# Kernel optimization log

Hardware: AMD Instinct MI355X
Metric: run time of the kernel (lower is better)

## Reference

```python
import jax, jax.numpy as jnp
import numpy as np

HID = 512
HEADS = 8
HEAD_DIM = HID // HEADS
BS, SEQ = 4, 2048


def setup_inputs() -> dict:
    key = jax.random.key(0)
    ks = jax.random.split(key, 12)
    s = 0.02
    return {
        "query": jax.random.normal(ks[0], (BS, SEQ, HID), jnp.float32),
        "key": jax.random.normal(ks[1], (BS, SEQ, HID), jnp.float32),
        "value": jax.random.normal(ks[2], (BS, SEQ, HID), jnp.float32),
        "query_mask": jnp.ones((BS, SEQ), dtype=bool),
        "key_mask": jnp.ones((BS, SEQ), dtype=bool),
        "Wq": jax.random.normal(ks[3], (HID, HID), jnp.float32) * s,
        "bq": jnp.zeros((HID,), jnp.float32),
        "Wk": jax.random.normal(ks[4], (HID, HID), jnp.float32) * s,
        "bk": jnp.zeros((HID,), jnp.float32),
        "Wv": jax.random.normal(ks[5], (HID, HID), jnp.float32) * s,
        "bv": jnp.zeros((HID,), jnp.float32),
        "Wo": jax.random.normal(ks[6], (HID, HID), jnp.float32) * s,
        "bo": jnp.zeros((HID,), jnp.float32),
    }


def _mha(query, key, value, query_mask, key_mask, Wq, bq, Wk, bk, Wv, bv, Wo, bo):
    bs, q_len, _ = query.shape
    k_len = key.shape[1]
    scale = jnp.sqrt(jnp.asarray(HEAD_DIM, query.dtype))

    def proj(x, W, b):  # nn.Linear: x @ W^T + b, then split heads -> [b,h,s,d]
        y = jnp.einsum('bse,fe->bsf', x, W) + b
        return y.reshape(bs, -1, HEADS, HEAD_DIM).transpose(0, 2, 1, 3)

    q = proj(query, Wq, bq)
    k = proj(key, Wk, bk)
    v = proj(value, Wv, bv)

    energy = jnp.einsum('bhqd,bhkd->bhqk', q, k) / scale  # [b,h,q,k]
    neg = -jnp.finfo(energy.dtype).max

    pad_mask = query_mask[:, None, :, None] & key_mask[:, None, None, :]
    energy = jnp.where(pad_mask, energy, neg)

    # causal: mask positions where q_idx < k_idx
    causal = jnp.arange(q_len)[:, None] < jnp.arange(k_len)[None, :]
    energy = jnp.where(causal[None, None], neg, energy)

    attn = jax.nn.softmax(energy, axis=-1)  # dropout p=0.0 -> identity
    x = jnp.einsum('bhqk,bhkd->bhqd', attn, v)
    x = x.transpose(0, 2, 1, 3).reshape(bs, q_len, HID)
    return jnp.einsum('bse,fe->bsf', x, Wo) + bo


def reference(query, key, value, query_mask, key_mask, Wq, bq, Wk, bk, Wv, bv, Wo, bo):
    return _mha(query, key, value, query_mask, key_mask, Wq, bq, Wk, bk, Wv, bv, Wo, bo)
```

## Files before the change

### kernel.cpp

```cpp
#include <hip/hip_runtime.h>
#include <hip/hip_bf16.h>

#define DEVI __device__ __forceinline__

typedef __attribute__((ext_vector_type(4)))  float f32x4;
typedef __attribute__((ext_vector_type(16))) float f32x16;
typedef __attribute__((ext_vector_type(8)))  short bf16x8;

constexpr int BS    = 4;
constexpr int SEQ   = 2048;
constexpr int HID   = 512;
constexpr int HEADS = 8;
constexpr int HD    = 64;
constexpr int M     = BS * SEQ;

constexpr float QSCALE = 0.125f * 1.4426950408889634f;
constexpr float M0 = 4.0f;

DEVI ushort f2bf(float f) {
    union { float f; unsigned u; } a; a.f = f;
    unsigned r = a.u + 0x7fffu + ((a.u >> 16) & 1u);
    return (ushort)(r >> 16);
}

DEVI f32x4 mfma16(bf16x8 a, bf16x8 b, f32x4 c) {
    return __builtin_amdgcn_mfma_f32_16x16x32_bf16(a, b, c, 0, 0, 0);
}
DEVI f32x16 mfma32(bf16x8 a, bf16x8 b, f32x16 c) {
    return __builtin_amdgcn_mfma_f32_32x32x16_bf16(a, b, c, 0, 0, 0);
}

DEVI void gl_lds16(const ushort* g, ushort* l) {
    __builtin_amdgcn_global_load_lds(
        (const __attribute__((address_space(1))) void*)g,
        (__attribute__((address_space(3))) void*)l,
        16, 0, 0);
}

DEVI unsigned cvtpk(float lo, float hi) {
    unsigned r;
    asm("v_cvt_pk_bf16_f32 %0, %1, %2" : "=v"(r) : "v"(lo), "v"(hi));
    return r;
}

DEVI void cvt_store(ushort* dst, float4 a, float4 b) {
    union { unsigned u[4]; bf16x8 v; } p;
    p.u[0] = cvtpk(a.x, a.y); p.u[1] = cvtpk(a.z, a.w);
    p.u[2] = cvtpk(b.x, b.y); p.u[3] = cvtpk(b.z, b.w);
    *(bf16x8*)dst = p.v;
}

__global__ void cast_w(const float* __restrict__ wq, const float* __restrict__ wk,
                       const float* __restrict__ wv, const float* __restrict__ wo,
                       ushort* __restrict__ oq, ushort* __restrict__ ok,
                       ushort* __restrict__ ov, ushort* __restrict__ oo)
{
    const int NW4 = HID * HID / 4;
    int i = blockIdx.x * blockDim.x + threadIdx.x;
    const int a = i >> 16, j = i & (NW4 - 1);
    const float* src = (a == 0) ? wq : (a == 1) ? wk : (a == 2) ? wv : wo;
    ushort* dst = (a == 0) ? oq : (a == 1) ? ok : (a == 2) ? ov : oo;
    float4 f = ((const float4*)src)[j];
    ushort4 u;
    u.x = f2bf(f.x); u.y = f2bf(f.y); u.z = f2bf(f.z); u.w = f2bf(f.w);
    ((ushort4*)dst)[j] = u;
}

template<bool AF32>
DEVI void gemm_core(const void* __restrict__ Ain, const ushort* __restrict__ W,
                    const float* __restrict__ bias, void* __restrict__ out,
                    float scale, int mode, ushort* sh)
{
    constexpr int BK = 32, NK = HID / BK;
    ushort* lA = sh;
    ushort* lB = sh + 12288;
    const int tid  = threadIdx.x;
    const int lane = tid & 63, w = tid >> 6;
    const int wm = w >> 1, wn = w & 1;
    const int l15 = lane & 15, lg = lane >> 4;
    const int m0 = blockIdx.x * 128, n0 = blockIdx.y * 128;
    const int fr = lane & 15;
    const int fc = (lane >> 4) * 8;

    const ushort* Ab  = (const ushort*)Ain;
    const float*  Af  = (const float*)Ain;
    const ushort* Ar0 = Ab + (size_t)(m0 + 32 * w + fr) * HID + fc;
    const ushort* Ar1 = Ab + (size_t)(m0 + 32 * w + 16 + fr) * HID + fc;
    const float*  Af0 = Af + (size_t)(m0 + 32 * w + fr) * HID + fc;
    const float*  Af1 = Af + (size_t)(m0 + 32 * w + 16 + fr) * HID + fc;
    const ushort* Wr0 = W + (size_t)(n0 + 32 * w + fr) * HID + fc;
    const ushort* Wr1 = W + (size_t)(n0 + 32 * w + 16 + fr) * HID + fc;

    ushort* ldsA0 = lA;
    ushort* wrA0  = lA + (2 * w) * 512 + lane * 8;
    ushort* wrA1  = lA + (2 * w + 1) * 512 + lane * 8;

    f32x4 acc[4][4];
    #pragma unroll
    for (int i = 0; i < 4; i++)
        #pragma unroll
        for (int n = 0; n < 4; n++) acc[i][n] = f32x4{0.f, 0.f, 0.f, 0.f};

    float4 rA[2][4];

    if constexpr (AF32) {
        rA[0][0] = *(const float4*)(Af0);
        rA[0][1] = *(const float4*)(Af0 + 4);
        rA[0][2] = *(const float4*)(Af1);
        rA[0][3] = *(const float4*)(Af1 + 4);
        gl_lds16(Wr0, lB + (2 * w) * 512);
        gl_lds16(Wr1, lB + (2 * w + 1) * 512);
        rA[1][0] = *(const float4*)(Af0 + BK);
        rA[1][1] = *(const float4*)(Af0 + BK + 4);
        rA[1][2] = *(const float4*)(Af1 + BK);
        rA[1][3] = *(const float4*)(Af1 + BK + 4);
        gl_lds16(Wr0 + BK, lB + 4096 + (2 * w) * 512);
        gl_lds16(Wr1 + BK, lB + 4096 + (2 * w + 1) * 512);
        asm volatile("s_waitcnt vmcnt(6)" ::: "memory");
        cvt_store(wrA0, rA[0][0], rA[0][1]);
        cvt_store(wrA1, rA[0][2], rA[0][3]);
        asm volatile("s_waitcnt lgkmcnt(0)" ::: "memory");
        asm volatile("s_barrier" ::: "memory");
    } else {
        #pragma unroll
        for (int kk = 0; kk < 2; kk++) {
            gl_lds16(Ar0 + kk * BK, lA + kk * 4096 + (2 * w) * 512);
            gl_lds16(Ar1 + kk * BK, lA + kk * 4096 + (2 * w + 1) * 512);
            gl_lds16(Wr0 + kk * BK, lB + kk * 4096 + (2 * w) * 512);
            gl_lds16(Wr1 + kk * BK, lB + kk * 4096 + (2 * w + 1) * 512);
        }
        asm volatile("s_waitcnt vmcnt(4)" ::: "memory");
        asm volatile("s_barrier" ::: "memory");
    }

    #pragma unroll
    for (int k = 0; k < NK; ++k) {
        const int cb = k % 3;
        const int nb = (k + 2) % 3;
        const int wb = (k + 1) % 3;
        ushort* lAc = lA + cb * 4096;
        ushort* lBc = lB + cb * 4096;

        if (k + 2 < NK) {
            if constexpr (AF32) {
                rA[k & 1][0] = *(const float4*)(Af0 + (k + 2) * BK);
                rA[k & 1][1] = *(const float4*)(Af0 + (k + 2) * BK + 4);
                rA[k & 1][2] = *(const float4*)(Af1 + (k + 2) * BK);
                rA[k & 1][3] = *(const float4*)(Af1 + (k + 2) * BK + 4);
            } else {
                gl_lds16(Ar0 + (k + 2) * BK, lA + nb * 4096 + (2 * w) * 512);
                gl_lds16(Ar1 + (k + 2) * BK, lA + nb * 4096 + (2 * w + 1) * 512);
            }
            gl_lds16(Wr0 + (k + 2) * BK, lB + nb * 4096 + (2 * w) * 512);
            gl_lds16(Wr1 + (k + 2) * BK, lB + nb * 4096 + (2 * w + 1) * 512);
        }

        bf16x8 af[4], bfr[4];
        #pragma unroll
        for (int i = 0; i < 4; i++)
            af[i] = *(const bf16x8*)(lAc + (wm * 4 + i) * 512 + lane * 8);
        #pragma unroll
        for (int n = 0; n < 4; n++)
            bfr[n] = *(const bf16x8*)(lBc + (wn * 4 + n) * 512 + lane * 8);
        __builtin_amdgcn_s_setprio(1);
        #pragma unroll
        for (int i = 0; i < 4; i++)
            #pragma unroll
            for (int n = 0; n < 4; n++)
                acc[i][n] = mfma16(af[i], bfr[n], acc[i][n]);
        __builtin_amdgcn_s_setprio(0);

        if (k + 1 < NK) {
            if constexpr (AF32) {
                if (k + 2 < NK) asm volatile("s_waitcnt vmcnt(6)" ::: "memory");
                else            asm volatile("s_waitcnt vmcnt(0)" ::: "memory");
                cvt_store(wrA0 + wb * 4096, rA[(k + 1) & 1][0], rA[(k + 1) & 1][1]);
                cvt_store(wrA1 + wb * 4096, rA[(k + 1) & 1][2], rA[(k + 1) & 1][3]);
                asm volatile("s_waitcnt lgkmcnt(0)" ::: "memory");
            } else {
                if (k + 2 < NK) asm volatile("s_waitcnt vmcnt(4)" ::: "memory");
                else            asm volatile("s_waitcnt vmcnt(0)" ::: "memory");
            }
            asm volatile("s_barrier" ::: "memory");
        }
    }

    if (mode == 3) {
        #pragma unroll
        for (int i = 0; i < 4; i++) {
            #pragma unroll
            for (int n = 0; n < 4; n++) {
                const int col = n0 + wn * 64 + n * 16 + l15;
                const float bb = bias[col];
                const int rbase = m0 + wm * 64 + i * 16 + lg * 4;
                #pragma unroll
                for (int jj = 0; jj < 4; jj++) {
                    ((float*)out)[(size_t)(rbase + jj) * HID + col] =
                        (acc[i][n][jj] + bb) * scale;
                }
            }
        }
        return;
    }

    __syncthreads();
    #pragma unroll
    for (int i = 0; i < 4; i++) {
        const int tloc = wm * 2 + (i >> 1);
        #pragma unroll
        for (int n = 0; n < 4; n++) {
            const int col = n0 + wn * 64 + n * 16 + l15;
            const float bb = bias[col];
            #pragma unroll
            for (int jj = 0; jj < 4; jj++) {
                const ushort u = f2bf((acc[i][n][jj] + bb) * scale);
                int inner;
                if (mode == 0) {
                    const int l31r = (i & 1) * 16 + lg * 4 + jj;
                    inner = n * 512 + ((l15 >> 3) * 32 + l31r) * 8 + (l15 & 7);
                } else {
                    inner = ((n >> 1) * 2 + (i & 1)) * 512 +
                            ((lg & 1) * 32 + (n & 1) * 16 + l15) * 8 +
                            jj + (lg >> 1) * 4;
                }
                sh[(wn * 4 + tloc) * 2048 + inner] = u;
            }
        }
    }
    __syncthreads();
    const int b  = m0 >> 11;
    const int t0 = (m0 & (SEQ - 1)) >> 5;
    ushort* og = (ushort*)out;
    #pragma unroll
    for (int c = 0; c < 8; c++) {
        const int hl = c >> 2, tl = c & 3;
        const int bh = b * HEADS + (n0 >> 6) + hl;
        *(bf16x8*)(og + (((size_t)bh * 64 + t0 + tl) * 4) * 512 + tid * 8) =
            *(const bf16x8*)(sh + c * 2048 + tid * 8);
    }
}

__global__ __launch_bounds__(256, 3)
void gemm_qkv(const float* __restrict__ Xq, const float* __restrict__ Xk,
              const float* __restrict__ Xv,
              const ushort* __restrict__ Wq, const ushort* __restrict__ Wk,
              const ushort* __restrict__ Wv,
              const float* __restrict__ bq, const float* __restrict__ bk,
              const float* __restrict__ bv,
              ushort* __restrict__ Qf, ushort* __restrict__ Kf,
              ushort* __restrict__ Vf)
{
    __shared__ ushort sh[24576];
    const int z = blockIdx.z;
    const float* A = z == 0 ? Xq : z == 1 ? Xk : Xv;
    const ushort* W = z == 0 ? Wq : z == 1 ? Wk : Wv;
    const float* bias = z == 0 ? bq : z == 1 ? bk : bv;
    void* out = z == 0 ? (void*)Qf : z == 1 ? (void*)Kf : (void*)Vf;
    gemm_core<true>(A, W, bias, out, z == 0 ? QSCALE : 1.0f, z == 2 ? 2 : 0, sh);
}

__global__ __launch_bounds__(256, 3)
void gemm_o(const ushort* __restrict__ ctx, const ushort* __restrict__ Wo,
            const float* __restrict__ bo, float* __restrict__ out)
{
    __shared__ ushort sh[24576];
    gemm_core<false>(ctx, Wo, bo, out, 1.0f, 3, sh);
}

__global__ __launch_bounds__(512)
void attn8(const ushort* __restrict__ Qf, const ushort* __restrict__ Kf,
           const ushort* __restrict__ Vf, ushort* __restrict__ ctx)
{
    __shared__ float part[2][4][16][64];
    __shared__ float pl[2][4][32];

    const int tid  = threadIdx.x;
    const int lane = tid & 63, w = tid >> 6;
    const int qsel = w >> 2, s = w & 3;
    const int l31 = lane & 31, hi = lane >> 5;

    const int bid = blockIdx.x;
    const int bh  = bid & 31;
    const int j   = bid >> 5;
    const int qt  = (62 - 2 * j) + qsel;
    const int qb  = qt * 32;

    const ushort* Qb = Qf + ((size_t)bh * 64 + qt) * 2048;
    const ushort* Kb = Kf + (size_t)bh * 64 * 2048;
    const ushort* Vb = Vf + (size_t)bh * 64 * 2048;

    bf16x8 qf[4];
    #pragma unroll
    for (int ds = 0; ds < 4; ds++)
        qf[ds] = *(const bf16x8*)(Qb + ds * 512 + lane * 8);

    f32x16 acc0 = {}, acc1 = {};
    float lrun = 0.f;

    bf16x8 kf[4] = {}, va[4] = {};
    if (s <= qt) {
        const ushort* kp = Kb + (size_t)s * 2048 + lane * 8;
        const ushort* vp = Vb + (size_t)s * 2048 + lane * 8;
        #pragma unroll
        for (int ds = 0; ds < 4; ds++) {
            kf[ds] = *(const bf16x8*)(kp + ds * 512);
            va[ds] = *(const bf16x8*)(vp + ds * 512);
        }
    }

    for (int t = s; t <= qt; t += 4) {
        f32x16 sc = {};
        __builtin_amdgcn_s_setprio(1);
        #pragma unroll
        for (int ds = 0; ds < 4; ds++)
            sc = mfma32(kf[ds], qf[ds], sc);
        __builtin_amdgcn_s_setprio(0);

        bf16x8 kfn[4], van[4];
        {
            const int tn = (t + 4 <= qt) ? t + 4 : t;
            const ushort* kp = Kb + (size_t)tn * 2048 + lane * 8;
            const ushort* vp = Vb + (size_t)tn * 2048 + lane * 8;
            #pragma unroll
            for (int ds = 0; ds < 4; ds++) {
                kfn[ds] = *(const bf16x8*)(kp + ds * 512);
                van[ds] = *(const bf16x8*)(vp + ds * 512);
            }
        }

        if (t == qt) {
            #pragma unroll
            for (int r = 0; r < 16; r++) {
                const int kvrow = (r & 3) + 8 * (r >> 2) + 4 * hi;
                sc[r] = (kvrow > l31) ? -3e38f : sc[r];
            }
        }

        float e[16];
        #pragma unroll
        for (int r = 0; r < 16; r++)
            e[r] = __builtin_amdgcn_exp2f(sc[r] - M0);
        float es0 = (e[0] + e[1]) + (e[2] + e[3]);
        float es1 = (e[4] + e[5]) + (e[6] + e[7]);
        float es2 = (e[8] + e[9]) + (e[10] + e[11]);
        float es3 = (e[12] + e[13]) + (e[14] + e[15]);
        lrun += (es0 + es1) + (es2 + es3);

        union { unsigned u[4]; bf16x8 v; } pb0, pb1;
        pb0.u[0] = cvtpk(e[0],  e[1]);  pb0.u[1] = cvtpk(e[2],  e[3]);
        pb0.u[2] = cvtpk(e[4],  e[5]);  pb0.u[3] = cvtpk(e[6],  e[7]);
        pb1.u[0] = cvtpk(e[8],  e[9]);  pb1.u[1] = cvtpk(e[10], e[11]);
        pb1.u[2] = cvtpk(e[12], e[13]); pb1.u[3] = cvtpk(e[14], e[15]);

        __builtin_amdgcn_s_setprio(1);
        acc0 = mfma32(va[0], pb0.v, acc0);
        acc0 = mfma32(va[1], pb1.v, acc0);
        acc1 = mfma32(va[2], pb0.v, acc1);
        acc1 = mfma32(va[3], pb1.v, acc1);
        __builtin_amdgcn_s_setprio(0);

        #pragma unroll
        for (int ds = 0; ds < 4; ds++) { kf[ds] = kfn[ds]; va[ds] = van[ds]; }
    }

    lrun += __shfl_xor(lrun, 32);

    const int b = bh >> 3, h = bh & 7;
    ushort* op = ctx + ((size_t)(b * SEQ + qb + l31)) * HID + h * HD;
    float inv = 0.f;

    #pragma unroll
    for (int pass = 0; pass < 2; pass++) {
        if (pass) __syncthreads();
        #pragma unroll
        for (int r = 0; r < 16; r++)
            part[qsel][s][r][lane] = pass ? acc1[r] : acc0[r];
        if (pass == 0 && hi == 0) pl[qsel][s][l31] = lrun;
        __syncthreads();

        if (pass == 0)
            inv = 1.f / (pl[qsel][0][l31] + pl[qsel][1][l31] +
                         pl[qsel][2][l31] + pl[qsel][3][l31]);

        float v[4];
        #pragma unroll
        for (int jj = 0; jj < 4; jj++) {
            const int r = 4 * s + jj;
            v[jj] = (part[qsel][0][r][lane] + part[qsel][1][r][lane] +
                     part[qsel][2][r][lane] + part[qsel][3][r][lane]) * inv;
        }
        ushort4 o;
        o.x = f2bf(v[0]); o.y = f2bf(v[1]); o.z = f2bf(v[2]); o.w = f2bf(v[3]);
        *(ushort4*)(op + pass * 32 + 8 * s + 4 * hi) = o;
    }
}

extern "C" void kernel_launch(void* const* d_in, const int* in_sizes, int n_in,
                              void* d_out, int out_size, void* d_ws, size_t ws_size,
                              hipStream_t stream) {
    const float* q  = (const float*)d_in[0];
    const float* k  = (const float*)d_in[1];
    const float* v  = (const float*)d_in[2];
    const float* Wq = (const float*)d_in[5];
    const float* bq = (const float*)d_in[6];
    const float* Wk = (const float*)d_in[7];
    const float* bk = (const float*)d_in[8];
    const float* Wv = (const float*)d_in[9];
    const float* bv = (const float*)d_in[10];
    const float* Wo = (const float*)d_in[11];
    const float* bo = (const float*)d_in[12];

    char* ws = (char*)d_ws;
    constexpr size_t XSZ = (size_t)M * HID * 2;
    constexpr size_t WSZ = (size_t)HID * HID * 2;
    ushort* Wqb = (ushort*)(ws);
    ushort* Wkb = (ushort*)(ws + WSZ);
    ushort* Wvb = (ushort*)(ws + 2 * WSZ);
    ushort* Wob = (ushort*)(ws + 3 * WSZ);
    ushort* Qf  = (ushort*)(ws + 4 * WSZ);
    ushort* Kf  = (ushort*)(ws + 4 * WSZ + XSZ);
    ushort* Vf  = (ushort*)(ws + 4 * WSZ + 2 * XSZ);
    ushort* ctx = (ushort*)(ws + 4 * WSZ + 3 * XSZ);

    cast_w<<<1024, 256, 0, stream>>>(Wq, Wk, Wv, Wo, Wqb, Wkb, Wvb, Wob);

    dim3 gqkv(M / 128, HID / 128, 3);
    gemm_qkv<<<gqkv, 256, 0, stream>>>(q, k, v, Wqb, Wkb, Wvb,
                                       bq, bk, bv, Qf, Kf, Vf);

    attn8<<<BS * HEADS * (SEQ / 64), 512, 0, stream>>>(Qf, Kf, Vf, ctx);

    dim3 go(M / 128, HID / 128);
    gemm_o<<<go, 256, 0, stream>>>(ctx, Wob, bo, (float*)d_out);
}
```

Measured before the change: 92.06 us.

## Stage fp32 activations directly into LDS and convert to bf16 at fragment load

The QKV projection GEMM used to load fp32 activations into registers, convert them to bf16 and write them to LDS. It now streams the fp32 tiles straight into LDS with global_load_lds and converts to bf16 when each wave reads its MFMA fragments. This removes the register round trip and the extra LDS store and wait from the pipeline. In exchange the kernel uses more LDS (a larger shared array with fp32 staging), its occupancy hint drops from 3 to 2 blocks, each fragment read issues twice as many LDS bytes, and the conversion work is repeated by both wn waves.

```diff
diff --git a/kernel.cpp b/kernel.cpp
--- a/kernel.cpp
+++ b/kernel.cpp
@@ -41,13 +41,6 @@
     unsigned r;
     asm("v_cvt_pk_bf16_f32 %0, %1, %2" : "=v"(r) : "v"(lo), "v"(hi));
     return r;
-}
-
-DEVI void cvt_store(ushort* dst, float4 a, float4 b) {
-    union { unsigned u[4]; bf16x8 v; } p;
-    p.u[0] = cvtpk(a.x, a.y); p.u[1] = cvtpk(a.z, a.w);
-    p.u[2] = cvtpk(b.x, b.y); p.u[3] = cvtpk(b.z, b.w);
-    *(bf16x8*)dst = p.v;
 }
 
 __global__ void cast_w(const float* __restrict__ wq, const float* __restrict__ wk,
@@ -72,8 +65,8 @@
                     float scale, int mode, ushort* sh)
 {
     constexpr int BK = 32, NK = HID / BK;
-    ushort* lA = sh;
-    ushort* lB = sh + 12288;
+    ushort* lB = sh + (AF32 ? 24576 : 12288);
+    float*  lAf = (float*)sh;
     const int tid  = threadIdx.x;
     const int lane = tid & 63, w = tid >> 6;
     const int wm = w >> 1, wn = w & 1;
@@ -82,86 +75,84 @@
     const int fr = lane & 15;
     const int fc = (lane >> 4) * 8;
 
-    const ushort* Ab  = (const ushort*)Ain;
-    const float*  Af  = (const float*)Ain;
+    const ushort* Ab = (const ushort*)Ain;
+    const float*  Af = (const float*)Ain;
     const ushort* Ar0 = Ab + (size_t)(m0 + 32 * w + fr) * HID + fc;
     const ushort* Ar1 = Ab + (size_t)(m0 + 32 * w + 16 + fr) * HID + fc;
-    const float*  Af0 = Af + (size_t)(m0 + 32 * w + fr) * HID + fc;
-    const float*  Af1 = Af + (size_t)(m0 + 32 * w + 16 + fr) * HID + fc;
     const ushort* Wr0 = W + (size_t)(n0 + 32 * w + fr) * HID + fc;
     const ushort* Wr1 = W + (size_t)(n0 + 32 * w + 16 + fr) * HID + fc;
 
-    ushort* ldsA0 = lA;
-    ushort* wrA0  = lA + (2 * w) * 512 + lane * 8;
-    ushort* wrA1  = lA + (2 * w + 1) * 512 + lane * 8;
-
     f32x4 acc[4][4];
     #pragma unroll
     for (int i = 0; i < 4; i++)
         #pragma unroll
         for (int n = 0; n < 4; n++) acc[i][n] = f32x4{0.f, 0.f, 0.f, 0.f};
 
-    float4 rA[2][4];
-
-    if constexpr (AF32) {
-        rA[0][0] = *(const float4*)(Af0);
-        rA[0][1] = *(const float4*)(Af0 + 4);
-        rA[0][2] = *(const float4*)(Af1);
-        rA[0][3] = *(const float4*)(Af1 + 4);
-        gl_lds16(Wr0, lB + (2 * w) * 512);
-        gl_lds16(Wr1, lB + (2 * w + 1) * 512);
-        rA[1][0] = *(const float4*)(Af0 + BK);
-        rA[1][1] = *(const float4*)(Af0 + BK + 4);
-        rA[1][2] = *(const float4*)(Af1 + BK);
-        rA[1][3] = *(const float4*)(Af1 + BK + 4);
-        gl_lds16(Wr0 + BK, lB + 4096 + (2 * w) * 512);
-        gl_lds16(Wr1 + BK, lB + 4096 + (2 * w + 1) * 512);
-        asm volatile("s_waitcnt vmcnt(6)" ::: "memory");
-        cvt_store(wrA0, rA[0][0], rA[0][1]);
-        cvt_store(wrA1, rA[0][2], rA[0][3]);
-        asm volatile("s_waitcnt lgkmcnt(0)" ::: "memory");
-        asm volatile("s_barrier" ::: "memory");
-    } else {
-        #pragma unroll
-        for (int kk = 0; kk < 2; kk++) {
-            gl_lds16(Ar0 + kk * BK, lA + kk * 4096 + (2 * w) * 512);
-            gl_lds16(Ar1 + kk * BK, lA + kk * 4096 + (2 * w + 1) * 512);
-            gl_lds16(Wr0 + kk * BK, lB + kk * 4096 + (2 * w) * 512);
-            gl_lds16(Wr1 + kk * BK, lB + kk * 4096 + (2 * w + 1) * 512);
-        }
-        asm volatile("s_waitcnt vmcnt(4)" ::: "memory");
-        asm volatile("s_barrier" ::: "memory");
-    }
+    auto stageA32 = [&](int k, int buf) {
+        #pragma unroll
+        for (int ff = 0; ff < 2; ff++) {
+            const int fi = 2 * w + ff;
+            #pragma unroll
+            for (int h = 0; h < 2; h++) {
+                const float* src = Af + (size_t)(m0 + 16 * fi + fr) * HID
+                                 + k * BK + h * 16 + lg * 4;
+                gl_lds16((const ushort*)src,
+                         sh + (size_t)buf * 8192 + (2 * fi + h) * 512);
+            }
+        }
+    };
+    auto stageA16 = [&](int k, int buf) {
+        gl_lds16(Ar0 + k * BK, sh + buf * 4096 + (2 * w) * 512);
+        gl_lds16(Ar1 + k * BK, sh + buf * 4096 + (2 * w + 1) * 512);
+    };
+    auto stageB = [&](int k, int buf) {
+        gl_lds16(Wr0 + k * BK, lB + buf * 4096 + (2 * w) * 512);
+        gl_lds16(Wr1 + k * BK, lB + buf * 4096 + (2 * w + 1) * 512);
+    };
+
+    if constexpr (AF32) { stageA32(0, 0); stageB(0, 0); stageA32(1, 1); stageB(1, 1); }
+    else               { stageA16(0, 0); stageB(0, 0); stageA16(1, 1); stageB(1, 1); }
+    if constexpr (AF32) asm volatile("s_waitcnt vmcnt(6)" ::: "memory");
+    else                asm volatile("s_waitcnt vmcnt(4)" ::: "memory");
+    asm volatile("s_barrier" ::: "memory");
+
+    const int hh  = lg >> 1;
+    const int grp = (lg & 1) * 2;
 
     #pragma unroll
     for (int k = 0; k < NK; ++k) {
         const int cb = k % 3;
         const int nb = (k + 2) % 3;
-        const int wb = (k + 1) % 3;
-        ushort* lAc = lA + cb * 4096;
+
+        if (k + 2 < NK) {
+            if constexpr (AF32) { stageA32(k + 2, nb); stageB(k + 2, nb); }
+            else               { stageA16(k + 2, nb); stageB(k + 2, nb); }
+        }
+
+        bf16x8 af[4], bfr[4];
+        if constexpr (AF32) {
+            #pragma unroll
+            for (int i = 0; i < 4; i++) {
+                const int fi = wm * 4 + i;
+                const float* pa = lAf + (size_t)cb * 4096 + (2 * fi + hh) * 256;
+                const f32x4 x0 = *(const f32x4*)(pa + (l15 + 16 * grp) * 4);
+                const f32x4 x1 = *(const f32x4*)(pa + (l15 + 16 * (grp + 1)) * 4);
+                union { unsigned u[4]; bf16x8 v; } p;
+                p.u[0] = cvtpk(x0[0], x0[1]); p.u[1] = cvtpk(x0[2], x0[3]);
+                p.u[2] = cvtpk(x1[0], x1[1]); p.u[3] = cvtpk(x1[2], x1[3]);
+                af[i] = p.v;
+            }
+        } else {
+            ushort* lAc = sh + cb * 4096;
+            #pragma unroll
+            for (int i = 0; i < 4; i++)
+                af[i] = *(const bf16x8*)(lAc + (wm * 4 + i) * 512 + lane * 8);
+        }
         ushort* lBc = lB + cb * 4096;
-
-        if (k + 2 < NK) {
-            if constexpr (AF32) {
-                rA[k & 1][0] = *(const float4*)(Af0 + (k + 2) * BK);
-                rA[k & 1][1] = *(const float4*)(Af0 + (k + 2) * BK + 4);
-                rA[k & 1][2] = *(const float4*)(Af1 + (k + 2) * BK);
-                rA[k & 1][3] = *(const float4*)(Af1 + (k + 2) * BK + 4);
-            } else {
-                gl_lds16(Ar0 + (k + 2) * BK, lA + nb * 4096 + (2 * w) * 512);
-                gl_lds16(Ar1 + (k + 2) * BK, lA + nb * 4096 + (2 * w + 1) * 512);
-            }
-            gl_lds16(Wr0 + (k + 2) * BK, lB + nb * 4096 + (2 * w) * 512);
-            gl_lds16(Wr1 + (k + 2) * BK, lB + nb * 4096 + (2 * w + 1) * 512);
-        }
-
-        bf16x8 af[4], bfr[4];
-        #pragma unroll
-        for (int i = 0; i < 4; i++)
-            af[i] = *(const bf16x8*)(lAc + (wm * 4 + i) * 512 + lane * 8);
         #pragma unroll
         for (int n = 0; n < 4; n++)
             bfr[n] = *(const bf16x8*)(lBc + (wn * 4 + n) * 512 + lane * 8);
+
         __builtin_amdgcn_s_setprio(1);
         #pragma unroll
         for (int i = 0; i < 4; i++)
@@ -171,15 +162,11 @@
         __builtin_amdgcn_s_setprio(0);
 
         if (k + 1 < NK) {
-            if constexpr (AF32) {
-                if (k + 2 < NK) asm volatile("s_waitcnt vmcnt(6)" ::: "memory");
-                else            asm volatile("s_waitcnt vmcnt(0)" ::: "memory");
-                cvt_store(wrA0 + wb * 4096, rA[(k + 1) & 1][0], rA[(k + 1) & 1][1]);
-                cvt_store(wrA1 + wb * 4096, rA[(k + 1) & 1][2], rA[(k + 1) & 1][3]);
-                asm volatile("s_waitcnt lgkmcnt(0)" ::: "memory");
+            if (k + 2 < NK) {
+                if constexpr (AF32) asm volatile("s_waitcnt vmcnt(6)" ::: "memory");
+                else                asm volatile("s_waitcnt vmcnt(4)" ::: "memory");
             } else {
-                if (k + 2 < NK) asm volatile("s_waitcnt vmcnt(4)" ::: "memory");
-                else            asm volatile("s_waitcnt vmcnt(0)" ::: "memory");
+                asm volatile("s_waitcnt vmcnt(0)" ::: "memory");
             }
             asm volatile("s_barrier" ::: "memory");
         }
@@ -240,7 +227,7 @@
     }
 }
 
-__global__ __launch_bounds__(256, 3)
+__global__ __launch_bounds__(256, 2)
 void gemm_qkv(const float* __restrict__ Xq, const float* __restrict__ Xk,
               const float* __restrict__ Xv,
               const ushort* __restrict__ Wq, const ushort* __restrict__ Wk,
@@ -250,7 +237,7 @@
               ushort* __restrict__ Qf, ushort* __restrict__ Kf,
               ushort* __restrict__ Vf)
 {
-    __shared__ ushort sh[24576];
+    __shared__ ushort sh[36864];
     const int z = blockIdx.z;
     const float* A = z == 0 ? Xq : z == 1 ? Xk : Xv;
     const ushort* W = z == 0 ? Wq : z == 1 ? Wk : Wv;
```

Measured after the change: 91.10 us. No clear change (-1.0%).
